# Kernel optimization log

Hardware: AMD Instinct MI355X
Metric: run time of the kernel (lower is better)

## Reference

```python
import jax, jax.numpy as jnp
import numpy as np

D_MODEL = 1024
NHEAD = 16
HEAD_DIM = D_MODEL // NHEAD


def setup_inputs() -> dict:
    key = jax.random.key(0)
    kx, kw1, kb1, kw2, kb2 = jax.random.split(key, 5)
    x = jax.random.normal(kx, (4, 2048, D_MODEL), dtype=jnp.float32)
    s = 1.0 / np.sqrt(D_MODEL)
    W_qkv = jax.random.uniform(kw1, (D_MODEL, 3 * D_MODEL), jnp.float32, -s, s)
    b_qkv = jax.random.uniform(kb1, (3 * D_MODEL,), jnp.float32, -s, s)
    W_out = jax.random.uniform(kw2, (D_MODEL, D_MODEL), jnp.float32, -s, s)
    b_out = jax.random.uniform(kb2, (D_MODEL,), jnp.float32, -s, s)
    return {"x": x, "W_qkv": W_qkv, "b_qkv": b_qkv, "W_out": W_out, "b_out": b_out}


def reference(x, W_qkv, b_qkv, W_out, b_out):
    B, S, _ = x.shape
    scale = HEAD_DIM ** -0.5
    qkv = x @ W_qkv + b_qkv                               # [B,S,3*D]
    qkv = qkv.reshape(B, S, 3, NHEAD, HEAD_DIM)
    qkv = jnp.transpose(qkv, (2, 0, 3, 1, 4))             # [3,B,H,S,Dh]
    q, k, v = qkv[0], qkv[1], qkv[2]
    scores = jnp.einsum('bhsd,bhtd->bhst', q, k) * scale  # [B,H,S,S]
    attn = jax.nn.softmax(scores, axis=-1)
    out = jnp.einsum('bhst,bhtd->bhsd', attn, v)          # [B,H,S,Dh]
    out = jnp.transpose(out, (0, 2, 1, 3)).reshape(B, S, D_MODEL)
    return out @ W_out + b_out
```

## Files before the change

kernel.cpp:

```cpp
#include <hip/hip_runtime.h>
#include <hip/hip_bf16.h>

#define SEQ 2048
#define BATCH 4
#define DMODEL 1024
#define NHEAD 16

#define QK_SCALE_LOG2E 0.1803368801111137f

typedef __attribute__((ext_vector_type(8))) __bf16 bf16x8;
typedef __attribute__((ext_vector_type(4))) __bf16 bf16x4;
typedef __attribute__((ext_vector_type(4))) float f32x4;

__device__ __forceinline__ void gload_lds16(const void* g, void* l) {
    __builtin_amdgcn_global_load_lds(
        (const __attribute__((address_space(1))) void*)g,
        (__attribute__((address_space(3))) void*)l, 16, 0, 0);
}

__global__ __launch_bounds__(256) void cast_f32_to_bf16(
    const float* __restrict__ in, __bf16* __restrict__ out, int n4)
{
    int i = blockIdx.x * 256 + threadIdx.x;
    if (i >= n4) return;
    float4 v = reinterpret_cast<const float4*>(in)[i];
    bf16x4 o = { (__bf16)v.x, (__bf16)v.y, (__bf16)v.z, (__bf16)v.w };
    reinterpret_cast<bf16x4*>(out)[i] = o;
}

__global__ __launch_bounds__(256) void trans_w(
    const float* __restrict__ W, __bf16* __restrict__ WT, int K, int N)
{
    __shared__ float t[32][33];
    const int tid = threadIdx.x;
    const int n0 = blockIdx.x * 32, k0 = blockIdx.y * 32;
    const int tx = tid & 31, ty = tid >> 5;
    #pragma unroll
    for (int j = 0; j < 4; ++j)
        t[ty + 8*j][tx] = W[(size_t)(k0 + ty + 8*j) * N + n0 + tx];
    __syncthreads();
    #pragma unroll
    for (int j = 0; j < 4; ++j)
        WT[(size_t)(n0 + ty + 8*j) * K + k0 + tx] = (__bf16)t[tx][ty + 8*j];
}

__global__ __launch_bounds__(256) void gemm_qkv(
    const __bf16* __restrict__ A, const __bf16* __restrict__ BT,
    const float* __restrict__ bias,
    __bf16* __restrict__ Qb, __bf16* __restrict__ Kt, __bf16* __restrict__ Vt,
    int M, int N, int K)
{
    __shared__ __attribute__((aligned(128))) char As[8192];
    __shared__ __attribute__((aligned(128))) char Bs[8192];

    const int tid = threadIdx.x, wv = tid >> 6, ln = tid & 63;
    const int nwg = gridDim.x * gridDim.y;
    const int bid = blockIdx.y * gridDim.x + blockIdx.x;
    const int swz = (bid & 7) * (nwg >> 3) + (bid >> 3);
    const int rowBase = (swz / gridDim.x) * 128;
    const int colBase = (swz % gridDim.x) * 128;

    const int mq = (wv >> 1) * 64, nq = (wv & 1) * 64;
    const int lg = ln >> 4, lc = ln & 15;
    const int srow = ln >> 2;
    const int skoff = (ln & 3) * 8;

    f32x4 acc[4][4] = {};

    for (int k0 = 0; k0 < K; k0 += 32) {
        __syncthreads();
        #pragma unroll
        for (int i = 0; i < 2; ++i) {
            int ch = wv * 2 + i;
            gload_lds16(A  + (size_t)(rowBase + ch*16 + srow) * K + k0 + skoff, As + ch*1024);
            gload_lds16(BT + (size_t)(colBase + ch*16 + srow) * K + k0 + skoff, Bs + ch*1024);
        }
        __syncthreads();

        bf16x8 af[4], bf[4];
        #pragma unroll
        for (int m = 0; m < 4; ++m)
            af[m] = *(const bf16x8*)(As + (mq + m*16 + lc) * 64 + lg * 16);
        #pragma unroll
        for (int n = 0; n < 4; ++n)
            bf[n] = *(const bf16x8*)(Bs + (nq + n*16 + lc) * 64 + lg * 16);
        #pragma unroll
        for (int m = 0; m < 4; ++m)
            #pragma unroll
            for (int n = 0; n < 4; ++n)
                acc[m][n] = __builtin_amdgcn_mfma_f32_16x16x32_bf16(af[m], bf[n], acc[m][n], 0, 0, 0);
    }

    #pragma unroll
    for (int m = 0; m < 4; ++m) {
        int row0 = rowBase + mq + m * 16 + lg * 4;
        int b = row0 >> 11, s0 = row0 & 2047;
        #pragma unroll
        for (int n = 0; n < 4; ++n) {
            int col = colBase + nq + n * 16 + lc;
            float bv = bias[col];
            if (colBase < DMODEL) {
                #pragma unroll
                for (int r = 0; r < 4; ++r)
                    Qb[(size_t)(row0 + r) * DMODEL + col] =
                        (__bf16)((acc[m][n][r] + bv) * QK_SCALE_LOG2E);
            } else if (colBase < 2 * DMODEL) {
                int h = (col >> 6) & 15, d = col & 63;
                __bf16* kp = &Kt[((size_t)(b * 16 + h) * SEQ + s0) * 64 + d];
                #pragma unroll
                for (int r = 0; r < 4; ++r)
                    kp[r * 64] = (__bf16)(acc[m][n][r] + bv);
            } else {
                int h = (col >> 6) & 15, d = col & 63;
                bf16x4 vv = { (__bf16)(acc[m][n][0] + bv), (__bf16)(acc[m][n][1] + bv),
                              (__bf16)(acc[m][n][2] + bv), (__bf16)(acc[m][n][3] + bv) };
                *(bf16x4*)&Vt[((size_t)(b * 16 + h) * 64 + d) * SEQ + s0] = vv;
            }
        }
    }
}

__global__ __launch_bounds__(256) void gemm_out(
    const __bf16* __restrict__ A, const __bf16* __restrict__ BT,
    const float* __restrict__ bias, float* __restrict__ Cout,
    int M, int N, int K)
{
    __shared__ __attribute__((aligned(128))) char As[8192];
    __shared__ __attribute__((aligned(128))) char Bs[8192];

    const int tid = threadIdx.x, wv = tid >> 6, ln = tid & 63;
    const int nwg = gridDim.x * gridDim.y;
    const int bid = blockIdx.y * gridDim.x + blockIdx.x;
    const int swz = (bid & 7) * (nwg >> 3) + (bid >> 3);
    const int rowBase = (swz / gridDim.x) * 128;
    const int colBase = (swz % gridDim.x) * 128;

    const int mq = (wv >> 1) * 64, nq = (wv & 1) * 64;
    const int lg = ln >> 4, lc = ln & 15;
    const int srow = ln >> 2;
    const int skoff = (ln & 3) * 8;

    f32x4 acc[4][4] = {};

    for (int k0 = 0; k0 < K; k0 += 32) {
        __syncthreads();
        #pragma unroll
        for (int i = 0; i < 2; ++i) {
            int ch = wv * 2 + i;
            gload_lds16(A  + (size_t)(rowBase + ch*16 + srow) * K + k0 + skoff, As + ch*1024);
            gload_lds16(BT + (size_t)(colBase + ch*16 + srow) * K + k0 + skoff, Bs + ch*1024);
        }
        __syncthreads();

        bf16x8 af[4], bf[4];
        #pragma unroll
        for (int m = 0; m < 4; ++m)
            af[m] = *(const bf16x8*)(As + (mq + m*16 + lc) * 64 + lg * 16);
        #pragma unroll
        for (int n = 0; n < 4; ++n)
            bf[n] = *(const bf16x8*)(Bs + (nq + n*16 + lc) * 64 + lg * 16);
        #pragma unroll
        for (int m = 0; m < 4; ++m)
            #pragma unroll
            for (int n = 0; n < 4; ++n)
                acc[m][n] = __builtin_amdgcn_mfma_f32_16x16x32_bf16(af[m], bf[n], acc[m][n], 0, 0, 0);
    }

    #pragma unroll
    for (int m = 0; m < 4; ++m) {
        int row0 = rowBase + mq + m * 16 + lg * 4;
        #pragma unroll
        for (int n = 0; n < 4; ++n) {
            int col = colBase + nq + n * 16 + lc;
            float bv = bias[col];
            #pragma unroll
            for (int r = 0; r < 4; ++r)
                Cout[(size_t)(row0 + r) * N + col] = acc[m][n][r] + bv;
        }
    }
}

__global__ __launch_bounds__(256, 3) void attn_mfma(
    const __bf16* __restrict__ Qb,
    const __bf16* __restrict__ Kt,
    const __bf16* __restrict__ Vt,
    __bf16* __restrict__ attn_out)
{
    __shared__ __attribute__((aligned(128))) char Ks[2][8192];
    __shared__ __attribute__((aligned(128))) char Vs[2][8192];
    __shared__ __attribute__((aligned(128))) char Ps[4][4096];

    const int tid = threadIdx.x, wv = tid >> 6, ln = tid & 63;
    const int swzb = (blockIdx.x & 7) * 128 + (blockIdx.x >> 3);
    const int qt = swzb & 15;
    const int bh = swzb >> 4;
    const int b = bh >> 4, h = bh & 15;
    const int lg = ln >> 4, lc = ln & 15;

    bf16x8 qf[2][2];
    #pragma unroll
    for (int m = 0; m < 2; ++m) {
        int qrow = qt * 128 + wv * 32 + m * 16 + lc;
        #pragma unroll
        for (int t = 0; t < 2; ++t)
            qf[m][t] = *(const bf16x8*)&Qb[((size_t)b * SEQ + qrow) * DMODEL + h * 64 + t * 32 + lg * 8];
    }

    f32x4 Oacc[4][2] = {};
    float lrun[2] = {0.f, 0.f};

    const int strow = ln >> 3;
    const int sl8 = ln & 7;
    const int r0 = (wv * 2 + 0) * 8 + strow;
    const int r1 = (wv * 2 + 1) * 8 + strow;
    const int s0 = sl8 ^ (r0 & 7);
    const int s1 = sl8 ^ (r1 & 7);
    const __bf16* ksrc0 = &Kt[((size_t)bh * SEQ + r0) * 64 + s0 * 8];
    const __bf16* ksrc1 = &Kt[((size_t)bh * SEQ + r1) * 64 + s1 * 8];
    const __bf16* vsrc0 = &Vt[((size_t)bh * 64 + r0) * SEQ + s0 * 8];
    const __bf16* vsrc1 = &Vt[((size_t)bh * 64 + r1) * SEQ + s1 * 8];

    #define STAGE(c, buf) do {                                                   \
        gload_lds16(ksrc0 + (size_t)(c) * 4096, Ks[buf] + (wv*2+0)*1024);        \
        gload_lds16(ksrc1 + (size_t)(c) * 4096, Ks[buf] + (wv*2+1)*1024);        \
        gload_lds16(vsrc0 + (size_t)(c) * 64,   Vs[buf] + (wv*2+0)*1024);        \
        gload_lds16(vsrc1 + (size_t)(c) * 64,   Vs[buf] + (wv*2+1)*1024);        \
    } while (0)

    STAGE(0, 0);
    STAGE(1, 1);

    char* PsW = Ps[wv];
    const int pxo = (lc & 7) << 4;

    for (int c = 0; c < SEQ / 64; ++c) {
        const int cur = c & 1;
        asm volatile("s_waitcnt vmcnt(4)" ::: "memory");
        __builtin_amdgcn_s_barrier();

        const char* Kc = Ks[cur];
        const char* Vc = Vs[cur];

        f32x4 Sacc[4][2] = {};
        #pragma unroll
        for (int n = 0; n < 4; ++n) {
            int row = n * 16 + lc;
            int xo = (row & 7) << 4;
            #pragma unroll
            for (int t = 0; t < 2; ++t) {
                bf16x8 kf = *(const bf16x8*)(Kc + row * 128 + ((t * 64 + lg * 16) ^ xo));
                #pragma unroll
                for (int m = 0; m < 2; ++m)
                    Sacc[n][m] = __builtin_amdgcn_mfma_f32_16x16x32_bf16(kf, qf[m][t], Sacc[n][m], 0, 0, 0);
            }
        }

        #pragma unroll
        for (int m = 0; m < 2; ++m) {
            float psum = 0.f;
            #pragma unroll
            for (int n = 0; n < 4; ++n) {
                float p0 = __builtin_amdgcn_exp2f(Sacc[n][m][0]);
                float p1 = __builtin_amdgcn_exp2f(Sacc[n][m][1]);
                float p2 = __builtin_amdgcn_exp2f(Sacc[n][m][2]);
                float p3 = __builtin_amdgcn_exp2f(Sacc[n][m][3]);
                psum += (p0 + p1) + (p2 + p3);
                bf16x4 pk = { (__bf16)p0, (__bf16)p1, (__bf16)p2, (__bf16)p3 };
                *(bf16x4*)(PsW + (m * 16 + lc) * 128 + (((n * 16 + lg * 4) * 2) ^ pxo)) = pk;
            }
            lrun[m] += psum;
        }

        #pragma unroll
        for (int t = 0; t < 2; ++t) {
            bf16x8 pf[2];
            #pragma unroll
            for (int m = 0; m < 2; ++m)
                pf[m] = *(const bf16x8*)(PsW + (m * 16 + lc) * 128 + ((t * 64 + lg * 16) ^ pxo));
            #pragma unroll
            for (int n = 0; n < 4; ++n) {
                int row = n * 16 + lc;
                bf16x8 vf = *(const bf16x8*)(Vc + row * 128 + ((t * 64 + lg * 16) ^ ((row & 7) << 4)));
                #pragma unroll
                for (int m = 0; m < 2; ++m)
                    Oacc[n][m] = __builtin_amdgcn_mfma_f32_16x16x32_bf16(vf, pf[m], Oacc[n][m], 0, 0, 0);
            }
        }

        __builtin_amdgcn_s_barrier();
        int cn = c + 2;
        if (cn > SEQ / 64 - 1) cn = SEQ / 64 - 1;
        STAGE(cn, cur);
    }
    asm volatile("s_waitcnt vmcnt(0)" ::: "memory");
    #undef STAGE

    #pragma unroll
    for (int m = 0; m < 2; ++m) {
        float l = lrun[m];
        l += __shfl_xor(l, 16);
        l += __shfl_xor(l, 32);
        float inv = 1.0f / l;
        int qrow = qt * 128 + wv * 32 + m * 16 + lc;
        #pragma unroll
        for (int n = 0; n < 4; ++n) {
            bf16x4 o = { (__bf16)(Oacc[n][m][0] * inv), (__bf16)(Oacc[n][m][1] * inv),
                         (__bf16)(Oacc[n][m][2] * inv), (__bf16)(Oacc[n][m][3] * inv) };
            *(bf16x4*)&attn_out[((size_t)b * SEQ + qrow) * DMODEL + h * 64 + n * 16 + lg * 4] = o;
        }
    }
}

extern "C" void kernel_launch(void* const* d_in, const int* in_sizes, int n_in,
                              void* d_out, int out_size, void* d_ws, size_t ws_size,
                              hipStream_t stream) {
    (void)in_sizes; (void)n_in; (void)out_size; (void)ws_size;
    const float* x     = (const float*)d_in[0];
    const float* W_qkv = (const float*)d_in[1];
    const float* b_qkv = (const float*)d_in[2];
    const float* W_out = (const float*)d_in[3];
    const float* b_out = (const float*)d_in[4];
    float* out = (float*)d_out;

    char* ws = (char*)d_ws;
    __bf16* xb    = (__bf16*)(ws);
    __bf16* WqkvT = (__bf16*)(ws + ((size_t)16 << 20));
    __bf16* WoutT = (__bf16*)(ws + ((size_t)22 << 20));
    __bf16* Qb    = (__bf16*)(ws + ((size_t)24 << 20));
    __bf16* Kt    = (__bf16*)(ws + ((size_t)40 << 20));
    __bf16* Vt    = (__bf16*)(ws + ((size_t)56 << 20));
    __bf16* attnb = (__bf16*)(ws + ((size_t)72 << 20));

    const int M = BATCH * SEQ;

    cast_f32_to_bf16<<<dim3(M * DMODEL / 4 / 256), 256, 0, stream>>>(x, xb, M * DMODEL / 4);
    trans_w<<<dim3(3 * DMODEL / 32, DMODEL / 32), 256, 0, stream>>>(W_qkv, WqkvT, DMODEL, 3 * DMODEL);
    trans_w<<<dim3(DMODEL / 32, DMODEL / 32), 256, 0, stream>>>(W_out, WoutT, DMODEL, DMODEL);

    gemm_qkv<<<dim3(3 * DMODEL / 128, M / 128), 256, 0, stream>>>(
        xb, WqkvT, b_qkv, Qb, Kt, Vt, M, 3 * DMODEL, DMODEL);

    attn_mfma<<<dim3(BATCH * NHEAD * (SEQ / 128)), 256, 0, stream>>>(Qb, Kt, Vt, attnb);

    gemm_out<<<dim3(DMODEL / 128, M / 128), 256, 0, stream>>>(
        attnb, WoutT, b_out, out, M, DMODEL, DMODEL);
}
```

Baseline: 201.8 us.

## Double-buffer LDS tiles in QKV and output GEMMs with async prefetch

Both projection GEMMs now keep two LDS buffers and issue global-to-LDS loads two k-tiles ahead, waiting with a partial vmcnt so only the current tile must have landed. The goal is to overlap global memory latency with the MFMA work instead of stalling at every k-step. The cost is double the LDS per block, which may lower occupancy, plus reliance on hand-placed waitcnt and barriers. The clamped last-tile reloads add a few redundant loads at the end of the loop.

```diff
diff --git a/kernel.cpp b/kernel.cpp
--- a/kernel.cpp
+++ b/kernel.cpp
@@ -50,8 +50,8 @@
     __bf16* __restrict__ Qb, __bf16* __restrict__ Kt, __bf16* __restrict__ Vt,
     int M, int N, int K)
 {
-    __shared__ __attribute__((aligned(128))) char As[8192];
-    __shared__ __attribute__((aligned(128))) char Bs[8192];
+    __shared__ __attribute__((aligned(128))) char As[2][8192];
+    __shared__ __attribute__((aligned(128))) char Bs[2][8192];
 
     const int tid = threadIdx.x, wv = tid >> 6, ln = tid & 63;
     const int nwg = gridDim.x * gridDim.y;
@@ -65,31 +65,49 @@
     const int srow = ln >> 2;
     const int skoff = (ln & 3) * 8;
 
+    const __bf16* asrc0 = A  + (size_t)(rowBase + (wv*2+0)*16 + srow) * K + skoff;
+    const __bf16* asrc1 = A  + (size_t)(rowBase + (wv*2+1)*16 + srow) * K + skoff;
+    const __bf16* bsrc0 = BT + (size_t)(colBase + (wv*2+0)*16 + srow) * K + skoff;
+    const __bf16* bsrc1 = BT + (size_t)(colBase + (wv*2+1)*16 + srow) * K + skoff;
+
+    #define GSTAGE(kt, buf) do {                                      \
+        gload_lds16(asrc0 + (kt) * 32, As[buf] + (wv*2+0)*1024);      \
+        gload_lds16(asrc1 + (kt) * 32, As[buf] + (wv*2+1)*1024);      \
+        gload_lds16(bsrc0 + (kt) * 32, Bs[buf] + (wv*2+0)*1024);      \
+        gload_lds16(bsrc1 + (kt) * 32, Bs[buf] + (wv*2+1)*1024);      \
+    } while (0)
+
+    const int nkt = K / 32;
+    GSTAGE(0, 0);
+    GSTAGE(1, 1);
+
     f32x4 acc[4][4] = {};
 
-    for (int k0 = 0; k0 < K; k0 += 32) {
-        __syncthreads();
-        #pragma unroll
-        for (int i = 0; i < 2; ++i) {
-            int ch = wv * 2 + i;
-            gload_lds16(A  + (size_t)(rowBase + ch*16 + srow) * K + k0 + skoff, As + ch*1024);
-            gload_lds16(BT + (size_t)(colBase + ch*16 + srow) * K + k0 + skoff, Bs + ch*1024);
-        }
-        __syncthreads();
+    for (int kt = 0; kt < nkt; ++kt) {
+        const int cur = kt & 1;
+        asm volatile("s_waitcnt vmcnt(4)" ::: "memory");
+        __builtin_amdgcn_s_barrier();
 
         bf16x8 af[4], bf[4];
         #pragma unroll
         for (int m = 0; m < 4; ++m)
-            af[m] = *(const bf16x8*)(As + (mq + m*16 + lc) * 64 + lg * 16);
+            af[m] = *(const bf16x8*)(As[cur] + (mq + m*16 + lc) * 64 + lg * 16);
         #pragma unroll
         for (int n = 0; n < 4; ++n)
-            bf[n] = *(const bf16x8*)(Bs + (nq + n*16 + lc) * 64 + lg * 16);
+            bf[n] = *(const bf16x8*)(Bs[cur] + (nq + n*16 + lc) * 64 + lg * 16);
         #pragma unroll
         for (int m = 0; m < 4; ++m)
             #pragma unroll
             for (int n = 0; n < 4; ++n)
                 acc[m][n] = __builtin_amdgcn_mfma_f32_16x16x32_bf16(af[m], bf[n], acc[m][n], 0, 0, 0);
-    }
+
+        __builtin_amdgcn_s_barrier();
+        int cn = kt + 2;
+        if (cn > nkt - 1) cn = nkt - 1;
+        GSTAGE(cn, cur);
+    }
+    asm volatile("s_waitcnt vmcnt(0)" ::: "memory");
+    #undef GSTAGE
 
     #pragma unroll
     for (int m = 0; m < 4; ++m) {
@@ -125,8 +143,8 @@
     const float* __restrict__ bias, float* __restrict__ Cout,
     int M, int N, int K)
 {
-    __shared__ __attribute__((aligned(128))) char As[8192];
-    __shared__ __attribute__((aligned(128))) char Bs[8192];
+    __shared__ __attribute__((aligned(128))) char As[2][8192];
+    __shared__ __attribute__((aligned(128))) char Bs[2][8192];
 
     const int tid = threadIdx.x, wv = tid >> 6, ln = tid & 63;
     const int nwg = gridDim.x * gridDim.y;
@@ -140,31 +158,49 @@
     const int srow = ln >> 2;
     const int skoff = (ln & 3) * 8;
 
+    const __bf16* asrc0 = A  + (size_t)(rowBase + (wv*2+0)*16 + srow) * K + skoff;
+    const __bf16* asrc1 = A  + (size_t)(rowBase + (wv*2+1)*16 + srow) * K + skoff;
+    const __bf16* bsrc0 = BT + (size_t)(colBase + (wv*2+0)*16 + srow) * K + skoff;
+    const __bf16* bsrc1 = BT + (size_t)(colBase + (wv*2+1)*16 + srow) * K + skoff;
+
+    #define GSTAGE(kt, buf) do {                                      \
+        gload_lds16(asrc0 + (kt) * 32, As[buf] + (wv*2+0)*1024);      \
+        gload_lds16(asrc1 + (kt) * 32, As[buf] + (wv*2+1)*1024);      \
+        gload_lds16(bsrc0 + (kt) * 32, Bs[buf] + (wv*2+0)*1024);      \
+        gload_lds16(bsrc1 + (kt) * 32, Bs[buf] + (wv*2+1)*1024);      \
+    } while (0)
+
+    const int nkt = K / 32;
+    GSTAGE(0, 0);
+    GSTAGE(1, 1);
+
     f32x4 acc[4][4] = {};
 
-    for (int k0 = 0; k0 < K; k0 += 32) {
-        __syncthreads();
-        #pragma unroll
-        for (int i = 0; i < 2; ++i) {
-            int ch = wv * 2 + i;
-            gload_lds16(A  + (size_t)(rowBase + ch*16 + srow) * K + k0 + skoff, As + ch*1024);
-            gload_lds16(BT + (size_t)(colBase + ch*16 + srow) * K + k0 + skoff, Bs + ch*1024);
-        }
-        __syncthreads();
+    for (int kt = 0; kt < nkt; ++kt) {
+        const int cur = kt & 1;
+        asm volatile("s_waitcnt vmcnt(4)" ::: "memory");
+        __builtin_amdgcn_s_barrier();
 
         bf16x8 af[4], bf[4];
         #pragma unroll
         for (int m = 0; m < 4; ++m)
-            af[m] = *(const bf16x8*)(As + (mq + m*16 + lc) * 64 + lg * 16);
+            af[m] = *(const bf16x8*)(As[cur] + (mq + m*16 + lc) * 64 + lg * 16);
         #pragma unroll
         for (int n = 0; n < 4; ++n)
-            bf[n] = *(const bf16x8*)(Bs + (nq + n*16 + lc) * 64 + lg * 16);
+            bf[n] = *(const bf16x8*)(Bs[cur] + (nq + n*16 + lc) * 64 + lg * 16);
         #pragma unroll
         for (int m = 0; m < 4; ++m)
             #pragma unroll
             for (int n = 0; n < 4; ++n)
                 acc[m][n] = __builtin_amdgcn_mfma_f32_16x16x32_bf16(af[m], bf[n], acc[m][n], 0, 0, 0);
-    }
+
+        __builtin_amdgcn_s_barrier();
+        int cn = kt + 2;
+        if (cn > nkt - 1) cn = nkt - 1;
+        GSTAGE(cn, cur);
+    }
+    asm volatile("s_waitcnt vmcnt(0)" ::: "memory");
+    #undef GSTAGE
 
     #pragma unroll
     for (int m = 0; m < 4; ++m) {
```

Result: no change. 197.9 us (-2.0%).
